# Performance work log

Hardware: AMD Instinct MI355X
Metric: run time of the kernel (lower is better)

The kernel has to match this reference:

```python
import jax, jax.numpy as jnp
import numpy as np

HEAD_DIM = 128

def setup_inputs() -> dict:
    key = jax.random.key(0)
    k1, k2, k3 = jax.random.split(key, 3)
    B, S, H, Hkv, D = 2, 2048, 32, 8, HEAD_DIM
    q = jax.random.normal(k1, (B, S, H, D), dtype=jnp.float32)
    k = jax.random.normal(k2, (B, S, Hkv, D), dtype=jnp.float32)
    v = jax.random.normal(k3, (B, S, Hkv, D), dtype=jnp.float32)
    return {"q": q, "k": k, "v": v}

def reference(q, k, v):
    # Causal GQA attention, same math as SDPA(is_causal=True, scale=head_dim**-0.5)
    # q: [B,S,H,D], k/v: [B,S,Hkv,D]; H = Hkv * G (grouped-query attention)
    B, S, H, D = q.shape
    Hkv = k.shape[2]
    G = H // Hkv
    scale = jnp.asarray(D, q.dtype) ** -0.5
    qg = q.reshape(B, S, Hkv, G, D)
    # scores: [B, Hkv, G, Sq, Sk]
    scores = jnp.einsum('bqhgd,bkhd->bhgqk', qg, k) * scale
    causal = jnp.tril(jnp.ones((S, S), dtype=bool))  # [Sq, Sk]
    scores = jnp.where(causal, scores, jnp.asarray(-jnp.inf, scores.dtype))
    probs = jax.nn.softmax(scores, axis=-1)
    out = jnp.einsum('bhgqk,bkhd->bqhgd', probs, v)
    return out.reshape(B, S, H, D)
```

## Files before the change

kernel.cpp:

```cpp
#include <hip/hip_runtime.h>
#include <hip/hip_bf16.h>

typedef short bf16x8 __attribute__((ext_vector_type(8)));
typedef float f32x4  __attribute__((ext_vector_type(4)));

#define B_    2
#define S_    2048
#define H_    32
#define HKV_  8
#define D_    128
#define QBLK  64
#define QBLK2 128
#define KVB   64
#define SCALE 0.1275431741f

static __device__ inline float exp2_fast(float x) {
    return __builtin_amdgcn_exp2f(x);
}

static __device__ inline unsigned short f2bf(float f) {
    unsigned u = __builtin_bit_cast(unsigned, f);
    u += 0x7fffu + ((u >> 16) & 1u);
    return (unsigned short)(u >> 16);
}
static __device__ inline unsigned pk2(float a, float b) {
    return (unsigned)f2bf(a) | ((unsigned)f2bf(b) << 16);
}
static __device__ inline short cvt_bf(float f) {
    __hip_bfloat16 h = __float2bfloat16(f);
    return __builtin_bit_cast(short, h);
}
static __device__ inline void gload16(const unsigned char* g, unsigned char* l) {
    __builtin_amdgcn_global_load_lds(
        (const __attribute__((address_space(1))) void*)g,
        (__attribute__((address_space(3))) void*)l, 16, 0, 0);
}

__global__ __launch_bounds__(256) void prep_k(const float* __restrict__ Kg,
                                              unsigned char* __restrict__ Kb) {
    const int s   = blockIdx.x * 256 + threadIdx.x;
    const int seg = s & 15;
    const int kv  = (s >> 4) & (S_ - 1);
    const int bhk = s >> 15;
    const int hk  = bhk & (HKV_ - 1);
    const int b   = bhk >> 3;
    const float* src = Kg + ((size_t)(b * S_ + kv) * HKV_ + hk) * D_ + seg * 8;
    float4 x0 = *(const float4*)(src);
    float4 x1 = *(const float4*)(src + 4);
    uint4 u = { pk2(x0.x, x0.y), pk2(x0.z, x0.w), pk2(x1.x, x1.y), pk2(x1.z, x1.w) };
    *(uint4*)(Kb + ((size_t)(b * HKV_ + hk) * S_ + kv) * 256 + ((seg * 16) ^ ((kv & 7) << 4))) = u;
}

__global__ __launch_bounds__(256) void prep_v(const float* __restrict__ Vg,
                                              unsigned short* __restrict__ Vb) {
    const int blk     = blockIdx.x;
    const int quarter = blk & 3;
    const int tile    = (blk >> 2) & 31;
    const int hk      = (blk >> 7) & (HKV_ - 1);
    const int b       = blk >> 10;
    const int t       = threadIdx.x;
    const int kp0     = (t & 7) * 8;
    const int d       = (t >> 3) + quarter * 32;
    const int kv0     = tile * KVB;
    unsigned short tmp[8];
#pragma unroll
    for (int j = 0; j < 8; ++j) {
        const int kp    = kp0 + j;
        const int chunk = kp >> 5;
        const int wi    = kp & 31;
        const int kv    = chunk * 32 + (((wi >> 2) & 1) << 4) + ((wi >> 3) << 2) + (wi & 3);
        tmp[j] = f2bf(Vg[((size_t)(b * S_ + kv0 + kv) * HKV_ + hk) * D_ + d]);
    }
    unsigned short* dst = Vb + ((size_t)(b * HKV_ + hk) * 32 + tile) * (128 * 80) + d * 80 + kp0;
    *(uint4*)dst = *(uint4*)tmp;
}

__global__ __launch_bounds__(256, 2) void fattn4(
        const float* __restrict__ Qg, const unsigned char* __restrict__ Kb,
        const unsigned char* __restrict__ Vb, float* __restrict__ Og) {
    __shared__ __align__(16) unsigned char lds[2 * 36864];

    const int tid  = threadIdx.x;
    const int lane = tid & 63;
    const int w    = tid >> 6;
    const int m    = lane & 15;
    const int g    = lane >> 4;
    const int lane16 = lane * 16;
    const int sw   = (m & 7) << 4;

    const int bid  = blockIdx.x;
    const int pair = bid >> 6;
    const int hb   = bid & 63;
    const int h    = hb & (H_ - 1);
    const int b    = hb >> 5;
    const int hk   = h >> 2;

    const unsigned char* KbH = Kb + (size_t)(b * HKV_ + hk) * S_ * 256;
    const unsigned char* VbH = Vb + (size_t)(b * HKV_ + hk) * 32 * 20480;
    const float* QgH = Qg + (size_t)(b * S_ * H_ + h) * D_;

#define STAGE(kt, cbuf) do {                                                  \
        const unsigned char* KbT = KbH + (size_t)(kt) * 16384;                \
        const unsigned char* VbT = VbH + (size_t)(kt) * 20480;                \
        unsigned char* dK = lds + (cbuf) * 36864;                             \
        unsigned char* dV = dK + 16384;                                       \
        gload16(KbT + (w * 4 + 0) * 1024 + lane16, dK + (w * 4 + 0) * 1024);  \
        gload16(KbT + (w * 4 + 1) * 1024 + lane16, dK + (w * 4 + 1) * 1024);  \
        gload16(KbT + (w * 4 + 2) * 1024 + lane16, dK + (w * 4 + 2) * 1024);  \
        gload16(KbT + (w * 4 + 3) * 1024 + lane16, dK + (w * 4 + 3) * 1024);  \
        gload16(VbT + (w * 5 + 0) * 1024 + lane16, dV + (w * 5 + 0) * 1024);  \
        gload16(VbT + (w * 5 + 1) * 1024 + lane16, dV + (w * 5 + 1) * 1024);  \
        gload16(VbT + (w * 5 + 2) * 1024 + lane16, dV + (w * 5 + 2) * 1024);  \
        gload16(VbT + (w * 5 + 3) * 1024 + lane16, dV + (w * 5 + 3) * 1024);  \
        gload16(VbT + (w * 5 + 4) * 1024 + lane16, dV + (w * 5 + 4) * 1024);  \
    } while (0)

    for (int job = 0; job < 2; ++job) {
        const int qt    = (job == 0) ? (15 - pair) : pair;
        const int qB    = qt * QBLK2;
        const int q0w   = qB + w * 32;
        const int qA    = q0w + m;
        const int qgate = q0w + 31;

        bf16x8 qfA[4], qfB[4];
        {
            const float* qrowA = QgH + (size_t)qA * H_ * D_;
            const float* qrowB = qrowA + (size_t)16 * H_ * D_;
#pragma unroll
            for (int db = 0; db < 4; ++db) {
                const float* pA = qrowA + db * 32 + g * 8;
                const float* pB = qrowB + db * 32 + g * 8;
                float4 a0 = *(const float4*)(pA);
                float4 a1 = *(const float4*)(pA + 4);
                float4 b0 = *(const float4*)(pB);
                float4 b1 = *(const float4*)(pB + 4);
                bf16x8 qa, qb;
                qa[0] = cvt_bf(a0.x * SCALE); qa[1] = cvt_bf(a0.y * SCALE);
                qa[2] = cvt_bf(a0.z * SCALE); qa[3] = cvt_bf(a0.w * SCALE);
                qa[4] = cvt_bf(a1.x * SCALE); qa[5] = cvt_bf(a1.y * SCALE);
                qa[6] = cvt_bf(a1.z * SCALE); qa[7] = cvt_bf(a1.w * SCALE);
                qb[0] = cvt_bf(b0.x * SCALE); qb[1] = cvt_bf(b0.y * SCALE);
                qb[2] = cvt_bf(b0.z * SCALE); qb[3] = cvt_bf(b0.w * SCALE);
                qb[4] = cvt_bf(b1.x * SCALE); qb[5] = cvt_bf(b1.y * SCALE);
                qb[6] = cvt_bf(b1.z * SCALE); qb[7] = cvt_bf(b1.w * SCALE);
                qfA[db] = qa; qfB[db] = qb;
            }
        }

        f32x4 oaccA[8], oaccB[8];
#pragma unroll
        for (int i = 0; i < 8; ++i) {
            oaccA[i] = (f32x4){0.f, 0.f, 0.f, 0.f};
            oaccB[i] = (f32x4){0.f, 0.f, 0.f, 0.f};
        }
        float m_run = 4.0f, lsumA = 0.f, lsumB = 0.f;

        const int nt = 2 * (qt + 1);
        int cur = 0;
        STAGE(0, 0);
        asm volatile("s_waitcnt vmcnt(0)" ::: "memory");
        __builtin_amdgcn_s_barrier();

        for (int t = 0; t < nt; ++t) {
            const int kv0 = t * KVB;
            if (t + 1 < nt) STAGE(t + 1, cur ^ 1);

            if (kv0 <= qgate) {
                const unsigned char* cK = lds + cur * 36864;
                const unsigned char* cV = cK + 16384;

                const f32x4 cinit = (f32x4){-m_run, -m_run, -m_run, -m_run};
                f32x4 sA[4], sB[4];
#pragma unroll
                for (int s = 0; s < 4; ++s) { sA[s] = cinit; sB[s] = cinit; }
                __builtin_amdgcn_s_setprio(1);
#pragma unroll
                for (int db = 0; db < 4; ++db) {
                    const int co = (db * 64 + g * 16) ^ sw;
#pragma unroll
                    for (int s = 0; s < 4; ++s) {
                        bf16x8 kf = *(const bf16x8*)(cK + (m + 16 * s) * 256 + co);
                        sA[s] = __builtin_amdgcn_mfma_f32_16x16x32_bf16(kf, qfA[db], sA[s], 0, 0, 0);
                        sB[s] = __builtin_amdgcn_mfma_f32_16x16x32_bf16(kf, qfB[db], sB[s], 0, 0, 0);
                    }
                }
                __builtin_amdgcn_s_setprio(0);

                if (kv0 + (KVB - 1) > q0w) {
                    const int qBrow = qA + 16;
#pragma unroll
                    for (int s = 0; s < 4; ++s)
#pragma unroll
                        for (int jj = 0; jj < 4; ++jj) {
                            const int kva = kv0 + 16 * s + g * 4 + jj;
                            if (kva > qA)    sA[s][jj] = -1e30f;
                            if (kva > qBrow) sB[s][jj] = -1e30f;
                        }
                }

                float pmax = -1e30f;
#pragma unroll
                for (int s = 0; s < 4; ++s)
#pragma unroll
                    for (int jj = 0; jj < 4; ++jj)
                        pmax = fmaxf(pmax, fmaxf(sA[s][jj], sB[s][jj]));
                if (__any(pmax > 12.0f)) {
                    float dm = fmaxf(pmax, __shfl_xor(pmax, 16));
                    dm = fmaxf(dm, __shfl_xor(dm, 32));
                    dm = fmaxf(dm, 0.0f);
                    const float corr = exp2_fast(-dm);
                    lsumA *= corr; lsumB *= corr;
                    float cj[4];
#pragma unroll
                    for (int jj = 0; jj < 4; ++jj) cj[jj] = __shfl(corr, g * 4 + jj);
#pragma unroll
                    for (int i = 0; i < 8; ++i)
#pragma unroll
                        for (int jj = 0; jj < 4; ++jj) {
                            oaccA[i][jj] *= cj[jj];
                            oaccB[i][jj] *= cj[jj];
                        }
                    m_run += dm;
#pragma unroll
                    for (int s = 0; s < 4; ++s)
#pragma unroll
                        for (int jj = 0; jj < 4; ++jj) {
                            sA[s][jj] -= dm; sB[s][jj] -= dm;
                        }
                }

#pragma unroll
                for (int s = 0; s < 4; ++s)
#pragma unroll
                    for (int jj = 0; jj < 4; ++jj) {
                        sA[s][jj] = exp2_fast(sA[s][jj]);
                        sB[s][jj] = exp2_fast(sB[s][jj]);
                    }
#pragma unroll
                for (int s = 0; s < 4; ++s) {
                    lsumA += (sA[s][0] + sA[s][1]) + (sA[s][2] + sA[s][3]);
                    lsumB += (sB[s][0] + sB[s][1]) + (sB[s][2] + sB[s][3]);
                }

                bf16x8 paA0, paA1, paB0, paB1;
#pragma unroll
                for (int jj = 0; jj < 4; ++jj) {
                    paA0[jj] = cvt_bf(sA[0][jj]); paA0[4 + jj] = cvt_bf(sA[1][jj]);
                    paA1[jj] = cvt_bf(sA[2][jj]); paA1[4 + jj] = cvt_bf(sA[3][jj]);
                    paB0[jj] = cvt_bf(sB[0][jj]); paB0[4 + jj] = cvt_bf(sB[1][jj]);
                    paB1[jj] = cvt_bf(sB[2][jj]); paB1[4 + jj] = cvt_bf(sB[3][jj]);
                }

                __builtin_amdgcn_s_setprio(1);
#pragma unroll
                for (int db8 = 0; db8 < 8; ++db8) {
                    const unsigned char* vrow = cV + (db8 * 16 + m) * 160 + g * 16;
                    bf16x8 vf0 = *(const bf16x8*)(vrow);
                    bf16x8 vf1 = *(const bf16x8*)(vrow + 64);
                    oaccA[db8] = __builtin_amdgcn_mfma_f32_16x16x32_bf16(paA0, vf0, oaccA[db8], 0, 0, 0);
                    oaccB[db8] = __builtin_amdgcn_mfma_f32_16x16x32_bf16(paB0, vf0, oaccB[db8], 0, 0, 0);
                    oaccA[db8] = __builtin_amdgcn_mfma_f32_16x16x32_bf16(paA1, vf1, oaccA[db8], 0, 0, 0);
                    oaccB[db8] = __builtin_amdgcn_mfma_f32_16x16x32_bf16(paB1, vf1, oaccB[db8], 0, 0, 0);
                }
                __builtin_amdgcn_s_setprio(0);
            }

            asm volatile("s_waitcnt vmcnt(0)" ::: "memory");
            __builtin_amdgcn_s_barrier();
            cur ^= 1;
        }

        lsumA += __shfl_xor(lsumA, 16); lsumA += __shfl_xor(lsumA, 32);
        lsumB += __shfl_xor(lsumB, 16); lsumB += __shfl_xor(lsumB, 32);
        const float rA = 1.0f / lsumA, rB = 1.0f / lsumB;
        float rsA[4], rsB[4];
#pragma unroll
        for (int jj = 0; jj < 4; ++jj) {
            rsA[jj] = __shfl(rA, g * 4 + jj);
            rsB[jj] = __shfl(rB, g * 4 + jj);
        }
#pragma unroll
        for (int db8 = 0; db8 < 8; ++db8) {
#pragma unroll
            for (int jj = 0; jj < 4; ++jj) {
                const int qrA = q0w + g * 4 + jj;
                Og[(size_t)((b * S_ + qrA) * H_ + h) * D_ + db8 * 16 + m]
                    = oaccA[db8][jj] * rsA[jj];
                Og[(size_t)((b * S_ + qrA + 16) * H_ + h) * D_ + db8 * 16 + m]
                    = oaccB[db8][jj] * rsB[jj];
            }
        }
    }
#undef STAGE
}

__global__ __launch_bounds__(256) void fattn_fallback(
        const float* __restrict__ Qg, const float* __restrict__ Kg,
        const float* __restrict__ Vg, float* __restrict__ Og) {
    __shared__ __align__(16) unsigned char  sK[32 * 256];
    __shared__ __align__(16) unsigned short sV[128 * 40];
    const int tid  = threadIdx.x;
    const int lane = tid & 63;
    const int w    = tid >> 6;
    const int m    = lane & 15;
    const int g    = lane >> 4;
    const int SQ = S_ / QBLK;
    const int bid = blockIdx.x;
    const int qt  = bid % SQ;
    const int h   = (bid / SQ) % H_;
    const int b   = bid / (SQ * H_);
    const int hk  = h >> 2;
    const int qB    = qt * QBLK;
    const int q0w   = qB + w * 16;
    const int q_abs = q0w + m;
    const float SC = 0.08838834764831845f;
    bf16x8 qf[4];
    {
        const float* qrow = Qg + (size_t)((b * S_ + q_abs) * H_ + h) * D_;
#pragma unroll
        for (int db = 0; db < 4; ++db) {
            const float* p = qrow + db * 32 + g * 8;
            float4 a = *(const float4*)(p);
            float4 c = *(const float4*)(p + 4);
            bf16x8 q8;
            q8[0] = (short)f2bf(a.x * SC); q8[1] = (short)f2bf(a.y * SC);
            q8[2] = (short)f2bf(a.z * SC); q8[3] = (short)f2bf(a.w * SC);
            q8[4] = (short)f2bf(c.x * SC); q8[5] = (short)f2bf(c.y * SC);
            q8[6] = (short)f2bf(c.z * SC); q8[7] = (short)f2bf(c.w * SC);
            qf[db] = q8;
        }
    }
    f32x4 oacc[8];
#pragma unroll
    for (int i = 0; i < 8; ++i) oacc[i] = (f32x4){0.f, 0.f, 0.f, 0.f};
    float m_run = -1e30f, lsum = 0.f;
    const int nt = (qB + QBLK) / 32;
    for (int t = 0; t < nt; ++t) {
        const int kv0 = t * 32;
        __syncthreads();
        {
            const int r = tid >> 3, seg = tid & 7;
            const float* src = Kg + (size_t)((b * S_ + kv0 + r) * HKV_ + hk) * D_ + seg * 16;
            float4 x0 = *(const float4*)(src + 0);
            float4 x1 = *(const float4*)(src + 4);
            float4 x2 = *(const float4*)(src + 8);
            float4 x3 = *(const float4*)(src + 12);
            uint4 u0 = { pk2(x0.x,x0.y), pk2(x0.z,x0.w), pk2(x1.x,x1.y), pk2(x1.z,x1.w) };
            uint4 u1 = { pk2(x2.x,x2.y), pk2(x2.z,x2.w), pk2(x3.x,x3.y), pk2(x3.z,x3.w) };
            const int colb = seg * 32;
            const int swz  = (r & 7) << 4;
            *(uint4*)(sK + r * 256 + ((colb     ) ^ swz)) = u0;
            *(uint4*)(sK + r * 256 + ((colb + 16) ^ swz)) = u1;
        }
        {
            const int kv = tid & 31, d0 = (tid >> 5) * 16;
            const int kp = (((kv & 15) >> 2) << 3) + ((kv >> 4) << 2) + (kv & 3);
            const float* src = Vg + (size_t)((b * S_ + kv0 + kv) * HKV_ + hk) * D_ + d0;
#pragma unroll
            for (int i = 0; i < 4; ++i) {
                float4 x = *(const float4*)(src + i * 4);
                const int d = d0 + i * 4;
                sV[(d + 0) * 40 + kp] = f2bf(x.x);
                sV[(d + 1) * 40 + kp] = f2bf(x.y);
                sV[(d + 2) * 40 + kp] = f2bf(x.z);
                sV[(d + 3) * 40 + kp] = f2bf(x.w);
            }
        }
        __syncthreads();
        if (kv0 > q0w + 15) continue;
        f32x4 st0 = (f32x4){0.f,0.f,0.f,0.f}, st1 = st0;
#pragma unroll
        for (int db = 0; db < 4; ++db) {
            const int swz = (m & 7) << 4;
            bf16x8 kf0 = *(const bf16x8*)(sK + (m      ) * 256 + ((db * 64 + g * 16) ^ swz));
            bf16x8 kf1 = *(const bf16x8*)(sK + (m + 16 ) * 256 + ((db * 64 + g * 16) ^ swz));
            st0 = __builtin_amdgcn_mfma_f32_16x16x32_bf16(kf0, qf[db], st0, 0, 0, 0);
            st1 = __builtin_amdgcn_mfma_f32_16x16x32_bf16(kf1, qf[db], st1, 0, 0, 0);
        }
        float p[8];
        float tm = -1e30f;
#pragma unroll
        for (int jj = 0; jj < 4; ++jj) {
            int kva = kv0 + g * 4 + jj;
            float s0 = (kva       <= q_abs) ? st0[jj] : -1e30f;
            float s1 = (kva + 16  <= q_abs) ? st1[jj] : -1e30f;
            p[jj]     = s0;
            p[4 + jj] = s1;
            tm = fmaxf(tm, fmaxf(s0, s1));
        }
        tm = fmaxf(tm, __shfl_xor(tm, 16));
        tm = fmaxf(tm, __shfl_xor(tm, 32));
        const float m_new = fmaxf(m_run, tm);
        const float corr  = __expf(m_run - m_new);
        float ls = 0.f;
#pragma unroll
        for (int i = 0; i < 8; ++i) { float e = __expf(p[i] - m_new); p[i] = e; ls += e; }
        ls += __shfl_xor(ls, 16);
        ls += __shfl_xor(ls, 32);
        lsum  = lsum * corr + ls;
        m_run = m_new;
        float cj[4];
#pragma unroll
        for (int jj = 0; jj < 4; ++jj) cj[jj] = __shfl(corr, g * 4 + jj);
#pragma unroll
        for (int i = 0; i < 8; ++i)
#pragma unroll
            for (int jj = 0; jj < 4; ++jj) oacc[i][jj] *= cj[jj];
        bf16x8 pa;
#pragma unroll
        for (int i = 0; i < 8; ++i) pa[i] = (short)f2bf(p[i]);
#pragma unroll
        for (int db8 = 0; db8 < 8; ++db8) {
            bf16x8 vf = *(const bf16x8*)((const unsigned char*)sV +
                          (((db8 * 16 + m) * 40 + g * 8) * 2));
            oacc[db8] = __builtin_amdgcn_mfma_f32_16x16x32_bf16(pa, vf, oacc[db8], 0, 0, 0);
        }
    }
    float rs[4];
    const float rinv = 1.0f / lsum;
#pragma unroll
    for (int jj = 0; jj < 4; ++jj) rs[jj] = __shfl(rinv, g * 4 + jj);
#pragma unroll
    for (int db8 = 0; db8 < 8; ++db8) {
#pragma unroll
        for (int jj = 0; jj < 4; ++jj) {
            const int qr = q0w + g * 4 + jj;
            Og[(size_t)((b * S_ + qr) * H_ + h) * D_ + db8 * 16 + m] = oacc[db8][jj] * rs[jj];
        }
    }
}

extern "C" void kernel_launch(void* const* d_in, const int* in_sizes, int n_in,
                              void* d_out, int out_size, void* d_ws, size_t ws_size,
                              hipStream_t stream) {
    const float* q = (const float*)d_in[0];
    const float* k = (const float*)d_in[1];
    const float* v = (const float*)d_in[2];
    float* o = (float*)d_out;

    const size_t KB_BYTES = (size_t)B_ * HKV_ * S_ * 256;
    const size_t VB_BYTES = (size_t)B_ * HKV_ * 32 * 128 * 80 * 2;

    if (ws_size >= KB_BYTES + VB_BYTES) {
        unsigned char*  Kb = (unsigned char*)d_ws;
        unsigned short* Vb = (unsigned short*)((unsigned char*)d_ws + KB_BYTES);
        prep_k<<<2048, 256, 0, stream>>>(k, Kb);
        prep_v<<<2048, 256, 0, stream>>>(v, Vb);
        fattn4<<<512, 256, 0, stream>>>(q, Kb, (const unsigned char*)Vb, o);
    } else {
        const int blocks = B_ * H_ * (S_ / QBLK);
        fattn_fallback<<<blocks, 256, 0, stream>>>(q, k, v, o);
    }
}
```

Before: 103.7 us.

## Split each warp's query rows across twice as many warps per block

The attention kernel moves from 4 warps each handling 32 query rows (two 16-row MFMA tiles) to 8 warps each handling 16 rows, with 512 threads per block. The K/V staging is redistributed over 8 warps. The goal is to halve per-warp accumulator registers, raise occupancy and parallelism, and hide latency. The cost is that each K/V fragment read from LDS is now reused for only one query tile instead of two, which doubles LDS read traffic per MFMA, and there are more warps contending at the barriers.

```diff
diff --git a/kernel.cpp b/kernel.cpp
--- a/kernel.cpp
+++ b/kernel.cpp
@@ -75,7 +75,7 @@
     *(uint4*)dst = *(uint4*)tmp;
 }
 
-__global__ __launch_bounds__(256, 2) void fattn4(
+__global__ __launch_bounds__(512, 4) void fattn5(
         const float* __restrict__ Qg, const unsigned char* __restrict__ Kb,
         const unsigned char* __restrict__ Vb, float* __restrict__ Og) {
     __shared__ __align__(16) unsigned char lds[2 * 36864];
@@ -104,56 +104,41 @@
         const unsigned char* VbT = VbH + (size_t)(kt) * 20480;                \
         unsigned char* dK = lds + (cbuf) * 36864;                             \
         unsigned char* dV = dK + 16384;                                       \
-        gload16(KbT + (w * 4 + 0) * 1024 + lane16, dK + (w * 4 + 0) * 1024);  \
-        gload16(KbT + (w * 4 + 1) * 1024 + lane16, dK + (w * 4 + 1) * 1024);  \
-        gload16(KbT + (w * 4 + 2) * 1024 + lane16, dK + (w * 4 + 2) * 1024);  \
-        gload16(KbT + (w * 4 + 3) * 1024 + lane16, dK + (w * 4 + 3) * 1024);  \
-        gload16(VbT + (w * 5 + 0) * 1024 + lane16, dV + (w * 5 + 0) * 1024);  \
-        gload16(VbT + (w * 5 + 1) * 1024 + lane16, dV + (w * 5 + 1) * 1024);  \
-        gload16(VbT + (w * 5 + 2) * 1024 + lane16, dV + (w * 5 + 2) * 1024);  \
-        gload16(VbT + (w * 5 + 3) * 1024 + lane16, dV + (w * 5 + 3) * 1024);  \
-        gload16(VbT + (w * 5 + 4) * 1024 + lane16, dV + (w * 5 + 4) * 1024);  \
+        gload16(KbT + (w * 2 + 0) * 1024 + lane16, dK + (w * 2 + 0) * 1024);  \
+        gload16(KbT + (w * 2 + 1) * 1024 + lane16, dK + (w * 2 + 1) * 1024);  \
+        gload16(VbT + (w * 2 + 0) * 1024 + lane16, dV + (w * 2 + 0) * 1024);  \
+        gload16(VbT + (w * 2 + 1) * 1024 + lane16, dV + (w * 2 + 1) * 1024);  \
+        if (w < 4) gload16(VbT + (16 + w) * 1024 + lane16, dV + (16 + w) * 1024); \
     } while (0)
 
     for (int job = 0; job < 2; ++job) {
         const int qt    = (job == 0) ? (15 - pair) : pair;
         const int qB    = qt * QBLK2;
-        const int q0w   = qB + w * 32;
+        const int q0w   = qB + w * 16;
         const int qA    = q0w + m;
-        const int qgate = q0w + 31;
-
-        bf16x8 qfA[4], qfB[4];
+        const int qgate = q0w + 15;
+
+        bf16x8 qf[4];
         {
-            const float* qrowA = QgH + (size_t)qA * H_ * D_;
-            const float* qrowB = qrowA + (size_t)16 * H_ * D_;
+            const float* qrow = QgH + (size_t)qA * H_ * D_;
 #pragma unroll
             for (int db = 0; db < 4; ++db) {
-                const float* pA = qrowA + db * 32 + g * 8;
-                const float* pB = qrowB + db * 32 + g * 8;
-                float4 a0 = *(const float4*)(pA);
-                float4 a1 = *(const float4*)(pA + 4);
-                float4 b0 = *(const float4*)(pB);
-                float4 b1 = *(const float4*)(pB + 4);
-                bf16x8 qa, qb;
+                const float* p = qrow + db * 32 + g * 8;
+                float4 a0 = *(const float4*)(p);
+                float4 a1 = *(const float4*)(p + 4);
+                bf16x8 qa;
                 qa[0] = cvt_bf(a0.x * SCALE); qa[1] = cvt_bf(a0.y * SCALE);
                 qa[2] = cvt_bf(a0.z * SCALE); qa[3] = cvt_bf(a0.w * SCALE);
                 qa[4] = cvt_bf(a1.x * SCALE); qa[5] = cvt_bf(a1.y * SCALE);
                 qa[6] = cvt_bf(a1.z * SCALE); qa[7] = cvt_bf(a1.w * SCALE);
-                qb[0] = cvt_bf(b0.x * SCALE); qb[1] = cvt_bf(b0.y * SCALE);
-                qb[2] = cvt_bf(b0.z * SCALE); qb[3] = cvt_bf(b0.w * SCALE);
-                qb[4] = cvt_bf(b1.x * SCALE); qb[5] = cvt_bf(b1.y * SCALE);
-                qb[6] = cvt_bf(b1.z * SCALE); qb[7] = cvt_bf(b1.w * SCALE);
-                qfA[db] = qa; qfB[db] = qb;
+                qf[db] = qa;
             }
         }
 
-        f32x4 oaccA[8], oaccB[8];
-#pragma unroll
-        for (int i = 0; i < 8; ++i) {
-            oaccA[i] = (f32x4){0.f, 0.f, 0.f, 0.f};
-            oaccB[i] = (f32x4){0.f, 0.f, 0.f, 0.f};
-        }
-        float m_run = 4.0f, lsumA = 0.f, lsumB = 0.f;
+        f32x4 oacc[8];
+#pragma unroll
+        for (int i = 0; i < 8; ++i) oacc[i] = (f32x4){0.f, 0.f, 0.f, 0.f};
+        float m_run = 4.0f, lsum = 0.f;
 
         const int nt = 2 * (qt + 1);
         int cur = 0;
@@ -170,9 +155,9 @@
                 const unsigned char* cV = cK + 16384;
 
                 const f32x4 cinit = (f32x4){-m_run, -m_run, -m_run, -m_run};
-                f32x4 sA[4], sB[4];
-#pragma unroll
-                for (int s = 0; s < 4; ++s) { sA[s] = cinit; sB[s] = cinit; }
+                f32x4 sA[4];
+#pragma unroll
+                for (int s = 0; s < 4; ++s) sA[s] = cinit;
                 __builtin_amdgcn_s_setprio(1);
 #pragma unroll
                 for (int db = 0; db < 4; ++db) {
@@ -180,21 +165,18 @@
 #pragma unroll
                     for (int s = 0; s < 4; ++s) {
                         bf16x8 kf = *(const bf16x8*)(cK + (m + 16 * s) * 256 + co);
-                        sA[s] = __builtin_amdgcn_mfma_f32_16x16x32_bf16(kf, qfA[db], sA[s], 0, 0, 0);
-                        sB[s] = __builtin_amdgcn_mfma_f32_16x16x32_bf16(kf, qfB[db], sB[s], 0, 0, 0);
+                        sA[s] = __builtin_amdgcn_mfma_f32_16x16x32_bf16(kf, qf[db], sA[s], 0, 0, 0);
                     }
                 }
                 __builtin_amdgcn_s_setprio(0);
 
                 if (kv0 + (KVB - 1) > q0w) {
-                    const int qBrow = qA + 16;
 #pragma unroll
                     for (int s = 0; s < 4; ++s)
 #pragma unroll
                         for (int jj = 0; jj < 4; ++jj) {
                             const int kva = kv0 + 16 * s + g * 4 + jj;
-                            if (kva > qA)    sA[s][jj] = -1e30f;
-                            if (kva > qBrow) sB[s][jj] = -1e30f;
+                            if (kva > qA) sA[s][jj] = -1e30f;
                         }
                 }
 
@@ -203,52 +185,40 @@
                 for (int s = 0; s < 4; ++s)
 #pragma unroll
                     for (int jj = 0; jj < 4; ++jj)
-                        pmax = fmaxf(pmax, fmaxf(sA[s][jj], sB[s][jj]));
+                        pmax = fmaxf(pmax, sA[s][jj]);
                 if (__any(pmax > 12.0f)) {
                     float dm = fmaxf(pmax, __shfl_xor(pmax, 16));
                     dm = fmaxf(dm, __shfl_xor(dm, 32));
                     dm = fmaxf(dm, 0.0f);
                     const float corr = exp2_fast(-dm);
-                    lsumA *= corr; lsumB *= corr;
+                    lsum *= corr;
                     float cj[4];
 #pragma unroll
                     for (int jj = 0; jj < 4; ++jj) cj[jj] = __shfl(corr, g * 4 + jj);
 #pragma unroll
                     for (int i = 0; i < 8; ++i)
 #pragma unroll
-                        for (int jj = 0; jj < 4; ++jj) {
-                            oaccA[i][jj] *= cj[jj];
-                            oaccB[i][jj] *= cj[jj];
-                        }
+                        for (int jj = 0; jj < 4; ++jj) oacc[i][jj] *= cj[jj];
                     m_run += dm;
 #pragma unroll
                     for (int s = 0; s < 4; ++s)
 #pragma unroll
-                        for (int jj = 0; jj < 4; ++jj) {
-                            sA[s][jj] -= dm; sB[s][jj] -= dm;
-                        }
+                        for (int jj = 0; jj < 4; ++jj) sA[s][jj] -= dm;
                 }
 
 #pragma unroll
                 for (int s = 0; s < 4; ++s)
 #pragma unroll
-                    for (int jj = 0; jj < 4; ++jj) {
-                        sA[s][jj] = exp2_fast(sA[s][jj]);
-                        sB[s][jj] = exp2_fast(sB[s][jj]);
-                    }
-#pragma unroll
-                for (int s = 0; s < 4; ++s) {
-                    lsumA += (sA[s][0] + sA[s][1]) + (sA[s][2] + sA[s][3]);
-                    lsumB += (sB[s][0] + sB[s][1]) + (sB[s][2] + sB[s][3]);
-                }
-
-                bf16x8 paA0, paA1, paB0, paB1;
+                    for (int jj = 0; jj < 4; ++jj) sA[s][jj] = exp2_fast(sA[s][jj]);
+#pragma unroll
+                for (int s = 0; s < 4; ++s)
+                    lsum += (sA[s][0] + sA[s][1]) + (sA[s][2] + sA[s][3]);
+
+                bf16x8 pa0, pa1;
 #pragma unroll
                 for (int jj = 0; jj < 4; ++jj) {
-                    paA0[jj] = cvt_bf(sA[0][jj]); paA0[4 + jj] = cvt_bf(sA[1][jj]);
-                    paA1[jj] = cvt_bf(sA[2][jj]); paA1[4 + jj] = cvt_bf(sA[3][jj]);
-                    paB0[jj] = cvt_bf(sB[0][jj]); paB0[4 + jj] = cvt_bf(sB[1][jj]);
-                    paB1[jj] = cvt_bf(sB[2][jj]); paB1[4 + jj] = cvt_bf(sB[3][jj]);
+                    pa0[jj] = cvt_bf(sA[0][jj]); pa0[4 + jj] = cvt_bf(sA[1][jj]);
+                    pa1[jj] = cvt_bf(sA[2][jj]); pa1[4 + jj] = cvt_bf(sA[3][jj]);
                 }
 
                 __builtin_amdgcn_s_setprio(1);
@@ -257,10 +227,8 @@
                     const unsigned char* vrow = cV + (db8 * 16 + m) * 160 + g * 16;
                     bf16x8 vf0 = *(const bf16x8*)(vrow);
                     bf16x8 vf1 = *(const bf16x8*)(vrow + 64);
-                    oaccA[db8] = __builtin_amdgcn_mfma_f32_16x16x32_bf16(paA0, vf0, oaccA[db8], 0, 0, 0);
-                    oaccB[db8] = __builtin_amdgcn_mfma_f32_16x16x32_bf16(paB0, vf0, oaccB[db8], 0, 0, 0);
-                    oaccA[db8] = __builtin_amdgcn_mfma_f32_16x16x32_bf16(paA1, vf1, oaccA[db8], 0, 0, 0);
-                    oaccB[db8] = __builtin_amdgcn_mfma_f32_16x16x32_bf16(paB1, vf1, oaccB[db8], 0, 0, 0);
+                    oacc[db8] = __builtin_amdgcn_mfma_f32_16x16x32_bf16(pa0, vf0, oacc[db8], 0, 0, 0);
+                    oacc[db8] = __builtin_amdgcn_mfma_f32_16x16x32_bf16(pa1, vf1, oacc[db8], 0, 0, 0);
                 }
                 __builtin_amdgcn_s_setprio(0);
             }
@@ -270,24 +238,19 @@
             cur ^= 1;
         }
 
-        lsumA += __shfl_xor(lsumA, 16); lsumA += __shfl_xor(lsumA, 32);
-        lsumB += __shfl_xor(lsumB, 16); lsumB += __shfl_xor(lsumB, 32);
-        const float rA = 1.0f / lsumA, rB = 1.0f / lsumB;
-        float rsA[4], rsB[4];
-#pragma unroll
-        for (int jj = 0; jj < 4; ++jj) {
-            rsA[jj] = __shfl(rA, g * 4 + jj);
-            rsB[jj] = __shfl(rB, g * 4 + jj);
-        }
+        lsum += __shfl_xor(lsum, 16);
+        lsum += __shfl_xor(lsum, 32);
+        const float rinv = 1.0f / lsum;
+        float rs[4];
+#pragma unroll
+        for (int jj = 0; jj < 4; ++jj) rs[jj] = __shfl(rinv, g * 4 + jj);
 #pragma unroll
         for (int db8 = 0; db8 < 8; ++db8) {
 #pragma unroll
             for (int jj = 0; jj < 4; ++jj) {
-                const int qrA = q0w + g * 4 + jj;
-                Og[(size_t)((b * S_ + qrA) * H_ + h) * D_ + db8 * 16 + m]
-                    = oaccA[db8][jj] * rsA[jj];
-                Og[(size_t)((b * S_ + qrA + 16) * H_ + h) * D_ + db8 * 16 + m]
-                    = oaccB[db8][jj] * rsB[jj];
+                const int qr = q0w + g * 4 + jj;
+                Og[(size_t)((b * S_ + qr) * H_ + h) * D_ + db8 * 16 + m]
+                    = oacc[db8][jj] * rs[jj];
             }
         }
     }
@@ -446,7 +409,7 @@
         unsigned short* Vb = (unsigned short*)((unsigned char*)d_ws + KB_BYTES);
         prep_k<<<2048, 256, 0, stream>>>(k, Kb);
         prep_v<<<2048, 256, 0, stream>>>(v, Vb);
-        fattn4<<<512, 256, 0, stream>>>(q, Kb, (const unsigned char*)Vb, o);
+        fattn5<<<512, 512, 0, stream>>>(q, Kb, (const unsigned char*)Vb, o);
     } else {
         const int blocks = B_ * H_ * (S_ / QBLK);
         fattn_fallback<<<blocks, 256, 0, stream>>>(q, k, v, o);
```

After: 110.0 us. +6.0%, slower.

## Split KV tile softmax/PV into halves, skip fully masked half, prefetch next job

Applied to the files above, without the earlier changes.

Processes each 64-key tile as two 32-key halves for the mask, softmax and PV MFMA stages, skipping the second half when it lies entirely above the causal diagonal for the warp. It also moves the initial KV stage out of the job loop so job 0's last iteration prefetches tile 0 for job 1, and reorders the QK loop to iterate over key subtiles outermost. The intent is to cut wasted MFMA and exp work on diagonal tiles and hide the job-transition load, at the cost of extra branching and duplicated rescale logic.

```diff
diff --git a/kernel.cpp b/kernel.cpp
--- a/kernel.cpp
+++ b/kernel.cpp
@@ -114,6 +114,38 @@
         gload16(VbT + (w * 5 + 3) * 1024 + lane16, dV + (w * 5 + 3) * 1024);  \
         gload16(VbT + (w * 5 + 4) * 1024 + lane16, dV + (w * 5 + 4) * 1024);  \
     } while (0)
+
+#define GUARD(pmaxv, S_LO, S_HI) do {                                         \
+        if (__any((pmaxv) > 12.0f)) {                                         \
+            float dm = fmaxf((pmaxv), __shfl_xor((pmaxv), 16));               \
+            dm = fmaxf(dm, __shfl_xor(dm, 32));                               \
+            dm = fmaxf(dm, 0.0f);                                             \
+            const float corr = exp2_fast(-dm);                                \
+            lsumA *= corr; lsumB *= corr;                                     \
+            float cj[4];                                                      \
+            _Pragma("unroll")                                                 \
+            for (int jj = 0; jj < 4; ++jj) cj[jj] = __shfl(corr, g * 4 + jj); \
+            _Pragma("unroll")                                                 \
+            for (int i = 0; i < 8; ++i)                                       \
+                _Pragma("unroll")                                             \
+                for (int jj = 0; jj < 4; ++jj) {                              \
+                    oaccA[i][jj] *= cj[jj];                                   \
+                    oaccB[i][jj] *= cj[jj];                                   \
+                }                                                             \
+            m_run += dm;                                                      \
+            _Pragma("unroll")                                                 \
+            for (int s = (S_LO); s < (S_HI); ++s)                             \
+                _Pragma("unroll")                                             \
+                for (int jj = 0; jj < 4; ++jj) {                              \
+                    sA[s][jj] -= dm; sB[s][jj] -= dm;                         \
+                }                                                             \
+        }                                                                     \
+    } while (0)
+
+    int cur = 0;
+    STAGE(0, 0);
+    asm volatile("s_waitcnt vmcnt(0)" ::: "memory");
+    __builtin_amdgcn_s_barrier();
 
     for (int job = 0; job < 2; ++job) {
         const int qt    = (job == 0) ? (15 - pair) : pair;
@@ -156,14 +188,11 @@
         float m_run = 4.0f, lsumA = 0.f, lsumB = 0.f;
 
         const int nt = 2 * (qt + 1);
-        int cur = 0;
-        STAGE(0, 0);
-        asm volatile("s_waitcnt vmcnt(0)" ::: "memory");
-        __builtin_amdgcn_s_barrier();
 
         for (int t = 0; t < nt; ++t) {
             const int kv0 = t * KVB;
-            if (t + 1 < nt) STAGE(t + 1, cur ^ 1);
+            if (t + 1 < nt)       STAGE(t + 1, cur ^ 1);
+            else if (job == 0)    STAGE(0, cur ^ 1);
 
             if (kv0 <= qgate) {
                 const unsigned char* cK = lds + cur * 36864;
@@ -175,10 +204,10 @@
                 for (int s = 0; s < 4; ++s) { sA[s] = cinit; sB[s] = cinit; }
                 __builtin_amdgcn_s_setprio(1);
 #pragma unroll
-                for (int db = 0; db < 4; ++db) {
-                    const int co = (db * 64 + g * 16) ^ sw;
-#pragma unroll
-                    for (int s = 0; s < 4; ++s) {
+                for (int s = 0; s < 4; ++s) {
+#pragma unroll
+                    for (int db = 0; db < 4; ++db) {
+                        const int co = (db * 64 + g * 16) ^ sw;
                         bf16x8 kf = *(const bf16x8*)(cK + (m + 16 * s) * 256 + co);
                         sA[s] = __builtin_amdgcn_mfma_f32_16x16x32_bf16(kf, qfA[db], sA[s], 0, 0, 0);
                         sB[s] = __builtin_amdgcn_mfma_f32_16x16x32_bf16(kf, qfB[db], sB[s], 0, 0, 0);
@@ -186,10 +215,10 @@
                 }
                 __builtin_amdgcn_s_setprio(0);
 
-                if (kv0 + (KVB - 1) > q0w) {
+                if (kv0 + 31 > q0w) {
                     const int qBrow = qA + 16;
 #pragma unroll
-                    for (int s = 0; s < 4; ++s)
+                    for (int s = 0; s < 2; ++s)
 #pragma unroll
                         for (int jj = 0; jj < 4; ++jj) {
                             const int kva = kv0 + 16 * s + g * 4 + jj;
@@ -197,58 +226,32 @@
                             if (kva > qBrow) sB[s][jj] = -1e30f;
                         }
                 }
-
-                float pmax = -1e30f;
-#pragma unroll
-                for (int s = 0; s < 4; ++s)
-#pragma unroll
-                    for (int jj = 0; jj < 4; ++jj)
-                        pmax = fmaxf(pmax, fmaxf(sA[s][jj], sB[s][jj]));
-                if (__any(pmax > 12.0f)) {
-                    float dm = fmaxf(pmax, __shfl_xor(pmax, 16));
-                    dm = fmaxf(dm, __shfl_xor(dm, 32));
-                    dm = fmaxf(dm, 0.0f);
-                    const float corr = exp2_fast(-dm);
-                    lsumA *= corr; lsumB *= corr;
-                    float cj[4];
-#pragma unroll
-                    for (int jj = 0; jj < 4; ++jj) cj[jj] = __shfl(corr, g * 4 + jj);
-#pragma unroll
-                    for (int i = 0; i < 8; ++i)
-#pragma unroll
-                        for (int jj = 0; jj < 4; ++jj) {
-                            oaccA[i][jj] *= cj[jj];
-                            oaccB[i][jj] *= cj[jj];
-                        }
-                    m_run += dm;
-#pragma unroll
-                    for (int s = 0; s < 4; ++s)
-#pragma unroll
-                        for (int jj = 0; jj < 4; ++jj) {
-                            sA[s][jj] -= dm; sB[s][jj] -= dm;
-                        }
-                }
-
-#pragma unroll
-                for (int s = 0; s < 4; ++s)
+                {
+                    float pmax = -1e30f;
+#pragma unroll
+                    for (int s = 0; s < 2; ++s)
+#pragma unroll
+                        for (int jj = 0; jj < 4; ++jj)
+                            pmax = fmaxf(pmax, fmaxf(sA[s][jj], sB[s][jj]));
+                    GUARD(pmax, 0, 4);
+                }
+#pragma unroll
+                for (int s = 0; s < 2; ++s)
 #pragma unroll
                     for (int jj = 0; jj < 4; ++jj) {
                         sA[s][jj] = exp2_fast(sA[s][jj]);
                         sB[s][jj] = exp2_fast(sB[s][jj]);
                     }
 #pragma unroll
-                for (int s = 0; s < 4; ++s) {
+                for (int s = 0; s < 2; ++s) {
                     lsumA += (sA[s][0] + sA[s][1]) + (sA[s][2] + sA[s][3]);
                     lsumB += (sB[s][0] + sB[s][1]) + (sB[s][2] + sB[s][3]);
                 }
-
-                bf16x8 paA0, paA1, paB0, paB1;
+                bf16x8 paA0, paB0;
 #pragma unroll
                 for (int jj = 0; jj < 4; ++jj) {
                     paA0[jj] = cvt_bf(sA[0][jj]); paA0[4 + jj] = cvt_bf(sA[1][jj]);
-                    paA1[jj] = cvt_bf(sA[2][jj]); paA1[4 + jj] = cvt_bf(sA[3][jj]);
                     paB0[jj] = cvt_bf(sB[0][jj]); paB0[4 + jj] = cvt_bf(sB[1][jj]);
-                    paB1[jj] = cvt_bf(sB[2][jj]); paB1[4 + jj] = cvt_bf(sB[3][jj]);
                 }
 
                 __builtin_amdgcn_s_setprio(1);
@@ -256,13 +259,60 @@
                 for (int db8 = 0; db8 < 8; ++db8) {
                     const unsigned char* vrow = cV + (db8 * 16 + m) * 160 + g * 16;
                     bf16x8 vf0 = *(const bf16x8*)(vrow);
-                    bf16x8 vf1 = *(const bf16x8*)(vrow + 64);
                     oaccA[db8] = __builtin_amdgcn_mfma_f32_16x16x32_bf16(paA0, vf0, oaccA[db8], 0, 0, 0);
                     oaccB[db8] = __builtin_amdgcn_mfma_f32_16x16x32_bf16(paB0, vf0, oaccB[db8], 0, 0, 0);
-                    oaccA[db8] = __builtin_amdgcn_mfma_f32_16x16x32_bf16(paA1, vf1, oaccA[db8], 0, 0, 0);
-                    oaccB[db8] = __builtin_amdgcn_mfma_f32_16x16x32_bf16(paB1, vf1, oaccB[db8], 0, 0, 0);
                 }
                 __builtin_amdgcn_s_setprio(0);
+
+                if (kv0 + 32 <= qgate) {
+                    if (kv0 + 63 > q0w) {
+                        const int qBrow = qA + 16;
+#pragma unroll
+                        for (int s = 2; s < 4; ++s)
+#pragma unroll
+                            for (int jj = 0; jj < 4; ++jj) {
+                                const int kva = kv0 + 16 * s + g * 4 + jj;
+                                if (kva > qA)    sA[s][jj] = -1e30f;
+                                if (kva > qBrow) sB[s][jj] = -1e30f;
+                            }
+                    }
+                    {
+                        float pmax = -1e30f;
+#pragma unroll
+                        for (int s = 2; s < 4; ++s)
+#pragma unroll
+                            for (int jj = 0; jj < 4; ++jj)
+                                pmax = fmaxf(pmax, fmaxf(sA[s][jj], sB[s][jj]));
+                        GUARD(pmax, 2, 4);
+                    }
+#pragma unroll
+                    for (int s = 2; s < 4; ++s)
+#pragma unroll
+                        for (int jj = 0; jj < 4; ++jj) {
+                            sA[s][jj] = exp2_fast(sA[s][jj]);
+                            sB[s][jj] = exp2_fast(sB[s][jj]);
+                        }
+#pragma unroll
+                    for (int s = 2; s < 4; ++s) {
+                        lsumA += (sA[s][0] + sA[s][1]) + (sA[s][2] + sA[s][3]);
+                        lsumB += (sB[s][0] + sB[s][1]) + (sB[s][2] + sB[s][3]);
+                    }
+                    bf16x8 paA1, paB1;
+#pragma unroll
+                    for (int jj = 0; jj < 4; ++jj) {
+                        paA1[jj] = cvt_bf(sA[2][jj]); paA1[4 + jj] = cvt_bf(sA[3][jj]);
+                        paB1[jj] = cvt_bf(sB[2][jj]); paB1[4 + jj] = cvt_bf(sB[3][jj]);
+                    }
+                    __builtin_amdgcn_s_setprio(1);
+#pragma unroll
+                    for (int db8 = 0; db8 < 8; ++db8) {
+                        const unsigned char* vrow = cV + (db8 * 16 + m) * 160 + g * 16;
+                        bf16x8 vf1 = *(const bf16x8*)(vrow + 64);
+                        oaccA[db8] = __builtin_amdgcn_mfma_f32_16x16x32_bf16(paA1, vf1, oaccA[db8], 0, 0, 0);
+                        oaccB[db8] = __builtin_amdgcn_mfma_f32_16x16x32_bf16(paB1, vf1, oaccB[db8], 0, 0, 0);
+                    }
+                    __builtin_amdgcn_s_setprio(0);
+                }
             }
 
             asm volatile("s_waitcnt vmcnt(0)" ::: "memory");
@@ -291,6 +341,7 @@
             }
         }
     }
+#undef GUARD
 #undef STAGE
 }
 
```

Result: slower. 107.0 us, median of 2 (+3.1%).
